# Optimization experiments

Hardware: AMD Instinct MI355X
Metric: run time of the kernel (lower is better)

The kernel has to match this reference:

```python
import jax, jax.numpy as jnp
import numpy as np

H = 256; NH = 8; DH = H // NH; L = 2; B = 32; S = 512; FIN = 199; A = 4


def _ln(x, g, b):
    m = jnp.mean(x, -1, keepdims=True)
    v = jnp.mean((x - m) ** 2, -1, keepdims=True)
    return (x - m) / jnp.sqrt(v + 1e-5) * g + b


def _grn(x, fc1w, fc1b, fc2w, fc2b, gw, gb, ggw, ggb, lg, lb):
    # GatedResidualNetwork, input_dim == output_dim so no skip layer, no context
    h = jax.nn.elu(x @ fc1w + fc1b)
    h = jax.nn.elu(h @ fc2w + fc2b)
    g = (h @ gw + gb) * jax.nn.sigmoid(h @ ggw + ggb)  # GLU
    return _ln(g + x, lg, lb)


def _attn(h, wq, bq, wk, bk, wv, bv, wo, bo):
    b, s, _ = h.shape
    q = (h @ wq + bq).reshape(b, s, NH, DH)
    k = (h @ wk + bk).reshape(b, s, NH, DH)
    v = (h @ wv + bv).reshape(b, s, NH, DH)
    scores = jnp.einsum('bqhd,bkhd->bhqk', q, k) / jnp.sqrt(jnp.float32(DH))
    mask = jnp.triu(jnp.ones((s, s), dtype=bool), 1)  # causal: mask strictly-future
    scores = jnp.where(mask, -jnp.inf, scores)
    aw = jax.nn.softmax(scores, axis=-1)
    ctx = jnp.einsum('bhqk,bkhd->bqhd', aw, v).reshape(b, s, H)
    return ctx @ wo + bo, aw


def _pe(s, d):
    pos = jnp.arange(s, dtype=jnp.float32)[:, None]
    div = jnp.exp(jnp.arange(0, d, 2, dtype=jnp.float32) * (-jnp.log(10000.0) / d))
    pe = jnp.zeros((s, d), dtype=jnp.float32)
    pe = pe.at[:, 0::2].set(jnp.sin(pos * div)).at[:, 1::2].set(jnp.cos(pos * div))
    return pe


def setup_inputs():
    key = jax.random.key(0)
    ks = iter(jax.random.split(key, 80))
    def nrm(shape, sc=0.02):
        return (jax.random.normal(next(ks), shape) * sc).astype(jnp.float32)
    d = {}
    d['x'] = jax.random.normal(next(ks), (B, S, FIN), dtype=jnp.float32)
    d['time_features'] = jax.random.normal(next(ks), (B, S, 3), dtype=jnp.float32)
    d['fp_w'] = nrm((FIN, H)); d['fp_b'] = jnp.zeros((H,), jnp.float32)
    d['tp_w'] = nrm((3, H));   d['tp_b'] = jnp.zeros((H,), jnp.float32)
    d['ip_w'] = nrm((H, H));   d['ip_b'] = jnp.zeros((H,), jnp.float32)
    for nm in ['wq', 'wk', 'wv', 'wo']:
        d[nm] = nrm((L, H, H))
    for nm in ['bq', 'bk', 'bv', 'bo']:
        d[nm] = jnp.zeros((L, H), jnp.float32)
    d['ln_g'] = jnp.ones((L, H), jnp.float32); d['ln_b'] = jnp.zeros((L, H), jnp.float32)
    for nm in ['g_fc1w', 'g_fc2w', 'g_gw', 'g_ggw']:
        d[nm] = nrm((L, H, H))
    for nm in ['g_fc1b', 'g_fc2b', 'g_gb', 'g_ggb']:
        d[nm] = jnp.zeros((L, H), jnp.float32)
    d['g_lg'] = jnp.ones((L, H), jnp.float32); d['g_lb'] = jnp.zeros((L, H), jnp.float32)
    for nm in ['f_fc1w', 'f_fc2w', 'f_gw', 'f_ggw']:
        d[nm] = nrm((H, H))
    for nm in ['f_fc1b', 'f_fc2b', 'f_gb', 'f_ggb']:
        d[nm] = jnp.zeros((H,), jnp.float32)
    d['f_lg'] = jnp.ones((H,), jnp.float32); d['f_lb'] = jnp.zeros((H,), jnp.float32)
    d['out_w'] = nrm((H, A)); d['out_b'] = jnp.zeros((A,), jnp.float32)
    return d


def reference(x, time_features, fp_w, fp_b, tp_w, tp_b, ip_w, ip_b,
              wq, bq, wk, bk, wv, bv, wo, bo, ln_g, ln_b,
              g_fc1w, g_fc1b, g_fc2w, g_fc2b, g_gw, g_gb, g_ggw, g_ggb, g_lg, g_lb,
              f_fc1w, f_fc1b, f_fc2w, f_fc2b, f_gw, f_gb, f_ggw, f_ggb, f_lg, f_lb,
              out_w, out_b):
    s = x.shape[1]
    hidden = (x @ fp_w + fp_b) + (time_features @ tp_w + tp_b)
    hidden = hidden @ ip_w + ip_b
    hidden = hidden + _pe(s, H)[None]
    aw = None
    for i in range(L):
        ao, aw = _attn(hidden, wq[i], bq[i], wk[i], bk[i], wv[i], bv[i], wo[i], bo[i])
        hidden = _ln(hidden + ao, ln_g[i], ln_b[i])
        hidden = _grn(hidden, g_fc1w[i], g_fc1b[i], g_fc2w[i], g_fc2b[i],
                      g_gw[i], g_gb[i], g_ggw[i], g_ggb[i], g_lg[i], g_lb[i])
    hidden = _grn(hidden, f_fc1w, f_fc1b, f_fc2w, f_fc2b, f_gw, f_gb, f_ggw, f_ggb, f_lg, f_lb)
    final = hidden[:, -1, :]
    logits = final @ out_w + out_b  # [B, A], one column per target asset
    return (logits, aw)
```

## Files before the change

kernel.cpp:

```cpp
#include <hip/hip_runtime.h>
#include <hip/hip_fp16.h>
#include <math.h>
#include <cstddef>

#define H 256
#define NH 8
#define DH 32
#define LAYERS 2
#define BB 32
#define SS 512
#define FINDIM 199
#define AA 4
#define T_TOK (BB*SS)
#define KIN 224
#define TPB 64

typedef unsigned short u16;
typedef unsigned int u32;
typedef __attribute__((ext_vector_type(8))) short short8;
typedef __attribute__((ext_vector_type(4))) float f4;

__device__ __forceinline__ float b2f(u16 v){
  unsigned u = ((unsigned)v) << 16;
  return __builtin_bit_cast(float, u);
}
__device__ __forceinline__ u16 f2b(float f){
  unsigned u = __builtin_bit_cast(unsigned, f);
  unsigned r = (u + 0x7fffu + ((u >> 16) & 1u)) >> 16;
  return (u16)r;
}
__device__ __forceinline__ float wave_sum(float v){
  #pragma unroll
  for (int mk=1; mk<64; mk<<=1) v += __shfl_xor(v, mk, 64);
  return v;
}

#define GLD_LDS16(g, l) \
  __builtin_amdgcn_global_load_lds((const __attribute__((address_space(1))) void*)(g), \
                                   (__attribute__((address_space(3))) void*)(l), 16, 0, 0)

#define SA (KIN+8)
#define SY (H+8)

template<int KC, int WK>
__device__ __forceinline__ void stage_acc64(
    const u16* Xl, int sx, const u16* __restrict__ Wt,
    int r0, int c0, int l16, int lq, f4 acc[2][4])
{
  #pragma unroll
  for (int mi=0;mi<2;mi++)
    #pragma unroll
    for (int ni=0;ni<4;ni++) acc[mi][ni] = (f4){0.f,0.f,0.f,0.f};
  #pragma unroll
  for (int kc=0;kc<KC;kc++){
    short8 af[2], bf[4];
    #pragma unroll
    for (int mi=0;mi<2;mi++)
      af[mi] = *(const short8*)&Xl[(r0 + mi*16 + l16)*sx + kc*32 + lq*8];
    #pragma unroll
    for (int ni=0;ni<4;ni++)
      bf[ni] = *(const short8*)(Wt + (size_t)(c0 + ni*16 + l16)*WK + kc*32 + lq*8);
    #pragma unroll
    for (int mi=0;mi<2;mi++)
      #pragma unroll
      for (int ni=0;ni<4;ni++)
        acc[mi][ni] = __builtin_amdgcn_mfma_f32_16x16x32_bf16(af[mi], bf[ni], acc[mi][ni], 0,0,0);
  }
}

template<int DO_ELU>
__device__ __forceinline__ void stage_store64(
    f4 acc[2][4], const float* __restrict__ bias,
    int r0, int c0, int l16, int lq, u16* Yl, int sy)
{
  #pragma unroll
  for (int ni=0;ni<4;ni++){
    int col = c0 + ni*16 + l16;
    float bc = bias[col];
    #pragma unroll
    for (int mi=0;mi<2;mi++){
      #pragma unroll
      for (int r=0;r<4;r++){
        int row = r0 + mi*16 + lq*4 + r;
        float v = acc[mi][ni][r] + bc;
        if (DO_ELU) v = v > 0.f ? v : expm1f(v);
        Yl[row*sy + col] = f2b(v);
      }
    }
  }
}

__device__ __forceinline__ void tile_load64(const u16* g, u16* Yl, int sy, int t){
  #pragma unroll
  for (int j=0;j<4;j++){
    int u = t + j*512;
    int row = u >> 5, cu = u & 31;
    *(short8*)&Yl[row*sy + cu*8] = *(const short8*)(g + (size_t)row*H + cu*8);
  }
}

template<int WB>
__device__ __forceinline__ void tile_ln64(
    u16* Yl, int sy, const float* __restrict__ g, const float* __restrict__ b,
    u16* out, int t)
{
  int w = t >> 6, lane = t & 63;
  #pragma unroll
  for (int rr=0;rr<8;rr++){
    int row = w*8 + rr;
    float xv[4];
    #pragma unroll
    for (int j=0;j<4;j++) xv[j] = b2f(Yl[row*sy + lane*4 + j]);
    float s=0.f, ss=0.f;
    #pragma unroll
    for (int j=0;j<4;j++){ s += xv[j]; ss += xv[j]*xv[j]; }
    s = wave_sum(s); ss = wave_sum(ss);
    float mean = s * (1.0f/H);
    float var  = ss * (1.0f/H) - mean*mean;
    float rstd = rsqrtf(var + 1e-5f);
    ushort4 o;
    int col = lane*4;
    o.x = f2b((xv[0]-mean)*rstd*g[col+0] + b[col+0]);
    o.y = f2b((xv[1]-mean)*rstd*g[col+1] + b[col+1]);
    o.z = f2b((xv[2]-mean)*rstd*g[col+2] + b[col+2]);
    o.w = f2b((xv[3]-mean)*rstd*g[col+3] + b[col+3]);
    *(ushort4*)(out + (size_t)row*H + col) = o;
    if (WB && row == 63) *(ushort4*)(Yl + row*sy + col) = o;
  }
}

struct WPtrs { const float* p[21]; };

__global__ __launch_bounds__(256) void wconv_kernel(WPtrs wp, u16* __restrict__ dst){
  __shared__ float tl[64][65];
  int mb = blockIdx.x >> 4, tile = blockIdx.x & 15;
  int k0 = (tile >> 2) * 64, n0 = (tile & 3) * 64;
  const float* src = wp.p[mb];
  int t = threadIdx.x;
  int r = t >> 4, cg = t & 15;
  #pragma unroll
  for (int p4=0;p4<4;p4++){
    f4 v = *(const f4*)(src + (size_t)(k0 + r + p4*16)*H + n0 + cg*4);
    tl[r+p4*16][cg*4+0]=v[0]; tl[r+p4*16][cg*4+1]=v[1];
    tl[r+p4*16][cg*4+2]=v[2]; tl[r+p4*16][cg*4+3]=v[3];
  }
  __syncthreads();
  u16* db = dst + (size_t)mb*H*H;
  #pragma unroll
  for (int p4=0;p4<4;p4++){
    int rn = r + p4*16;
    ushort4 o;
    o.x = f2b(tl[cg*4+0][rn]); o.y = f2b(tl[cg*4+1][rn]);
    o.z = f2b(tl[cg*4+2][rn]); o.w = f2b(tl[cg*4+3][rn]);
    *(ushort4*)(db + (size_t)(n0+rn)*H + k0 + cg*4) = o;
  }
}

__global__ __launch_bounds__(256) void wcat_kernel(
    const float* __restrict__ fp_w, const float* __restrict__ tp_w,
    u16* __restrict__ wcat){
  int idx = blockIdx.x*256 + threadIdx.x;
  if (idx >= 256*KIN) return;
  int n = idx / KIN, k2 = idx % KIN;
  float v = 0.f;
  if (k2 < FINDIM) v = fp_w[(size_t)k2*H + n];
  else if (k2 < FINDIM+3) v = tp_w[(size_t)(k2-FINDIM)*H + n];
  wcat[idx] = f2b(v);
}

__global__ __launch_bounds__(256) void xconv_kernel(
    const float* __restrict__ x, const float* __restrict__ tf,
    u16* __restrict__ ab){
  size_t idx = (size_t)blockIdx.x*256 + threadIdx.x;
  if (idx >= (size_t)T_TOK*KIN) return;
  int tok = idx / KIN, k2 = idx % KIN;
  float v = 0.f;
  if (k2 < FINDIM) v = x[(size_t)tok*FINDIM + k2];
  else if (k2 < FINDIM+3) v = tf[(size_t)tok*3 + (k2-FINDIM)];
  ab[idx] = f2b(v);
}

__global__ __launch_bounds__(512,2) void input_kernel(
    const u16* __restrict__ ab, const u16* __restrict__ wcat,
    const float* __restrict__ fp_b, const float* __restrict__ tp_b,
    const u16* __restrict__ ipw, const float* __restrict__ ip_b,
    u16* __restrict__ hid){
  __shared__ u16 Al[TPB*SA];
  __shared__ u16 Tl[TPB*SY];
  int t = threadIdx.x;
  int tok0 = blockIdx.x * TPB;
  int lane = t & 63, w = t >> 6;
  int l16 = lane & 15, lq = lane >> 4;
  int r0 = (w >> 2) * 32;
  int c0 = (w & 3) * 64;

  #pragma unroll
  for (int j=0;j<4;j++){
    int u = t + j*512;
    if (u < 1792){
      int row = u / 28, cu = u % 28;
      *(short8*)&Al[row*SA + cu*8] = *(const short8*)(ab + (size_t)(tok0+row)*KIN + cu*8);
    }
  }
  __syncthreads();

  f4 acc[2][4];
  stage_acc64<7, KIN>(Al, SA, wcat, r0, c0, l16, lq, acc);
  #pragma unroll
  for (int ni=0;ni<4;ni++){
    int col = c0 + ni*16 + l16;
    float bc = fp_b[col] + tp_b[col];
    #pragma unroll
    for (int mi=0;mi<2;mi++)
      #pragma unroll
      for (int r=0;r<4;r++){
        int row = r0 + mi*16 + lq*4 + r;
        Tl[row*SY + col] = f2b(acc[mi][ni][r] + bc);
      }
  }
  __syncthreads();

  stage_acc64<8, H>(Tl, SY, ipw, r0, c0, l16, lq, acc);
  #pragma unroll
  for (int ni=0;ni<4;ni++){
    int col = c0 + ni*16 + l16;
    float bc = ip_b[col];
    int ii = col >> 1;
    float div = __expf((float)(2*ii) * -0.03597789207803197f);
    #pragma unroll
    for (int mi=0;mi<2;mi++)
      #pragma unroll
      for (int r=0;r<4;r++){
        int row = r0 + mi*16 + lq*4 + r;
        int s = (tok0 + row) & (SS-1);
        float arg = (float)s * div;
        float pe = (col & 1) ? cosf(arg) : sinf(arg);
        hid[(size_t)(tok0+row)*H + col] = f2b(acc[mi][ni][r] + bc + pe);
      }
  }
}

__global__ __launch_bounds__(512,2) void oproj_ln_kernel(
    const u16* __restrict__ ctx, u16* __restrict__ hid,
    const u16* __restrict__ wo, const float* __restrict__ bo,
    const float* __restrict__ g, const float* __restrict__ b){
  __shared__ u16 Xl[TPB*SY];
  __shared__ u16 Rl[TPB*SY];
  int t = threadIdx.x;
  int tok0 = blockIdx.x * TPB;
  int lane = t & 63, w = t >> 6;
  int l16 = lane & 15, lq = lane >> 4;
  int r0 = (w >> 2) * 32;
  int c0 = (w & 3) * 64;
  u16* hb = hid + (size_t)tok0*H;

  tile_load64(ctx + (size_t)tok0*H, Xl, SY, t);
  tile_load64(hb, Rl, SY, t);
  __syncthreads();

  f4 acc[2][4];
  stage_acc64<8, H>(Xl, SY, wo, r0, c0, l16, lq, acc);
  __syncthreads();
  #pragma unroll
  for (int ni=0;ni<4;ni++){
    int col = c0 + ni*16 + l16;
    float bc = bo[col];
    #pragma unroll
    for (int mi=0;mi<2;mi++)
      #pragma unroll
      for (int r=0;r<4;r++){
        int row = r0 + mi*16 + lq*4 + r;
        float y = acc[mi][ni][r] + bc + b2f(Rl[row*SY + col]);
        Xl[row*SY + col] = f2b(y);
      }
  }
  __syncthreads();
  tile_ln64<0>(Xl, SY, g, b, hb, t);
}

template<int LOGITS>
__global__ __launch_bounds__(512,2) void grn_kernel(
    u16* __restrict__ hid,
    const u16* __restrict__ fc1, const u16* __restrict__ fc2,
    const u16* __restrict__ gw,  const u16* __restrict__ ggw,
    const float* __restrict__ b1, const float* __restrict__ b2,
    const float* __restrict__ gb, const float* __restrict__ ggb,
    const float* __restrict__ lg, const float* __restrict__ lb,
    const float* __restrict__ ow, const float* __restrict__ ob,
    float* __restrict__ lout){
  __shared__ u16 Xa[TPB*SY];
  __shared__ u16 Xb[TPB*SY];
  int t = threadIdx.x;
  int tok0 = blockIdx.x * TPB;
  int lane = t & 63, w = t >> 6;
  int l16 = lane & 15, lq = lane >> 4;
  int r0 = (w >> 2) * 32;
  int c0 = (w & 3) * 64;
  u16* hb = hid + (size_t)tok0*H;

  tile_load64(hb, Xa, SY, t);
  __syncthreads();

  f4 acc[2][4];
  stage_acc64<8, H>(Xa, SY, fc1, r0, c0, l16, lq, acc);
  stage_store64<1>(acc, b1, r0, c0, l16, lq, Xb, SY);
  __syncthreads();
  stage_acc64<8, H>(Xb, SY, fc2, r0, c0, l16, lq, acc);
  __syncthreads();
  stage_store64<1>(acc, b2, r0, c0, l16, lq, Xb, SY);
  __syncthreads();

  stage_acc64<8, H>(Xb, SY, ggw, r0, c0, l16, lq, acc);
  u32 sgp[2][4][2];
  #pragma unroll
  for (int mi=0;mi<2;mi++)
    #pragma unroll
    for (int ni=0;ni<4;ni++){
      float bc = ggb[c0 + ni*16 + l16];
      float s0 = 1.0f/(1.0f + __expf(-(acc[mi][ni][0]+bc)));
      float s1 = 1.0f/(1.0f + __expf(-(acc[mi][ni][1]+bc)));
      float s2 = 1.0f/(1.0f + __expf(-(acc[mi][ni][2]+bc)));
      float s3 = 1.0f/(1.0f + __expf(-(acc[mi][ni][3]+bc)));
      sgp[mi][ni][0] = __builtin_bit_cast(u32, __floats2half2_rn(s0, s1));
      sgp[mi][ni][1] = __builtin_bit_cast(u32, __floats2half2_rn(s2, s3));
    }

  stage_acc64<8, H>(Xb, SY, gw, r0, c0, l16, lq, acc);
  __syncthreads();
  #pragma unroll
  for (int ni=0;ni<4;ni++){
    int col = c0 + ni*16 + l16;
    float bc = gb[col];
    #pragma unroll
    for (int mi=0;mi<2;mi++){
      float2 s01 = __half22float2(__builtin_bit_cast(__half2, sgp[mi][ni][0]));
      float2 s23 = __half22float2(__builtin_bit_cast(__half2, sgp[mi][ni][1]));
      float sv[4] = {s01.x, s01.y, s23.x, s23.y};
      #pragma unroll
      for (int r=0;r<4;r++){
        int row = r0 + mi*16 + lq*4 + r;
        float y = (acc[mi][ni][r] + bc) * sv[r] + b2f(Xa[row*SY + col]);
        Xb[row*SY + col] = f2b(y);
      }
    }
  }
  __syncthreads();
  tile_ln64<LOGITS>(Xb, SY, lg, lb, hb, t);

  if (LOGITS){
    if ((tok0 & (SS-1)) == SS - TPB){
      __syncthreads();
      if (t < 64){
        int bidx = tok0 >> 9;
        float a0=0.f, a1=0.f, a2=0.f, a3=0.f;
        #pragma unroll
        for (int j=0;j<4;j++){
          int k = t*4 + j;
          float xv = b2f(Xb[63*SY + k]);
          f4 wr = *(const f4*)(ow + (size_t)k*AA);
          a0 = fmaf(xv, wr[0], a0);
          a1 = fmaf(xv, wr[1], a1);
          a2 = fmaf(xv, wr[2], a2);
          a3 = fmaf(xv, wr[3], a3);
        }
        a0 = wave_sum(a0); a1 = wave_sum(a1);
        a2 = wave_sum(a2); a3 = wave_sum(a3);
        if (t == 0){
          lout[bidx*AA+0] = a0 + ob[0];
          lout[bidx*AA+1] = a1 + ob[1];
          lout[bidx*AA+2] = a2 + ob[2];
          lout[bidx*AA+3] = a3 + ob[3];
        }
      }
    }
  }
}

struct GemmJob  { const u16* Wt; const float* bias; u16* C; };
struct GemmBatch{ GemmJob j[3]; };

__global__ __launch_bounds__(256) void gemm_bf16(
    const u16* __restrict__ A, GemmBatch jb) {
  __shared__ u16 smem[128*64 + 64*64];
  u16* As  = smem;
  u16* Wsm = smem + 128*64;
  const GemmJob job = jb.j[blockIdx.z];
  const u16* Wt = job.Wt;
  int t = threadIdx.x;
  int m0 = blockIdx.x * 128;
  int n0 = blockIdx.y * 64;
  int lane = t & 63, w = t >> 6;
  int wr = (w >> 1) * 64;
  int wc = (w & 1) * 32;
  int l16 = lane & 15, lq = lane >> 4;

  f4 acc[4][2];
  #pragma unroll
  for (int mi=0;mi<4;mi++)
    #pragma unroll
    for (int ni=0;ni<2;ni++) acc[mi][ni] = (f4){0.f,0.f,0.f,0.f};

  for (int k0=0;k0<256;k0+=64){
    #pragma unroll
    for (int ja=0;ja<4;ja++){
      int ub = (w*4 + ja)*64;
      int u  = ub + lane;
      int m  = u >> 3, c = u & 7, kx = c ^ (m & 7);
      const u16* g = A + (size_t)(m0+m)*H + k0 + kx*8;
      GLD_LDS16(g, As + (size_t)ub*8);
    }
    #pragma unroll
    for (int jb2=0;jb2<2;jb2++){
      int ub = (w*2 + jb2)*64;
      int u  = ub + lane;
      int n  = u >> 3, c = u & 7, kx = c ^ (n & 7);
      const u16* g = Wt + (size_t)(n0+n)*H + k0 + kx*8;
      GLD_LDS16(g, Wsm + (size_t)ub*8);
    }
    __syncthreads();
    #pragma unroll
    for (int kc=0;kc<2;kc++){
      short8 af[4], bf[2];
      int kx = kc*4 + lq;
      #pragma unroll
      for (int mi=0;mi<4;mi++){
        int m = wr + mi*16 + l16;
        int un = (m<<3) | (kx ^ (m&7));
        af[mi] = *(short8*)&As[un*8];
      }
      #pragma unroll
      for (int ni=0;ni<2;ni++){
        int n = wc + ni*16 + l16;
        int un = (n<<3) | (kx ^ (n&7));
        bf[ni] = *(short8*)&Wsm[un*8];
      }
      #pragma unroll
      for (int mi=0;mi<4;mi++)
        #pragma unroll
        for (int ni=0;ni<2;ni++)
          acc[mi][ni] = __builtin_amdgcn_mfma_f32_16x16x32_bf16(af[mi], bf[ni], acc[mi][ni], 0,0,0);
    }
    __syncthreads();
  }

  u16* Cl = smem;
  #pragma unroll
  for (int ni=0;ni<2;ni++){
    int coll = wc + ni*16 + l16;
    float bcol = job.bias[n0 + coll];
    #pragma unroll
    for (int mi=0;mi<4;mi++){
      #pragma unroll
      for (int r=0;r<4;r++){
        int rowl = wr + mi*16 + lq*4 + r;
        Cl[rowl*68 + coll] = f2b(acc[mi][ni][r] + bcol);
      }
    }
  }
  __syncthreads();
  #pragma unroll
  for (int q2=0;q2<4;q2++){
    int u = q2*256 + t;
    int row = u >> 3, cu = u & 7;
    short8 val = *(short8*)&Cl[row*68 + cu*8];
    *(short8*)(job.C + (size_t)(m0+row)*H + n0 + cu*8) = val;
  }
}

template<int WRITE_AW>
__global__ __launch_bounds__(256) void attn_kernel(
    const u16* __restrict__ q, const u16* __restrict__ k,
    const u16* __restrict__ v, float* __restrict__ aw,
    u16* __restrict__ ctx) {
  __shared__ u16 Vt[DH][SS+8];
  __shared__ u16 Plds[4][16][72];
  int t  = threadIdx.x;
  int qt = blockIdx.x;
  int bh = blockIdx.y;
  int b  = bh >> 3, h = bh & 7;
  int lane = t & 63, w = t >> 6;
  int l16 = lane & 15, lq = lane >> 4;
  const float scale = 0.17677669529663687f;

  int nrows = (qt+1)*64;
  for (int kk = t; kk < nrows; kk += 256){
    const u16* vp = v + ((size_t)(b*SS + kk))*H + h*DH;
    short8 r0v = *(const short8*)(vp);
    short8 r1v = *(const short8*)(vp+8);
    short8 r2v = *(const short8*)(vp+16);
    short8 r3v = *(const short8*)(vp+24);
    #pragma unroll
    for (int j=0;j<8;j++){
      Vt[j][kk]    = (u16)r0v[j];
      Vt[8+j][kk]  = (u16)r1v[j];
      Vt[16+j][kk] = (u16)r2v[j];
      Vt[24+j][kk] = (u16)r3v[j];
    }
  }
  __syncthreads();

  {
    int qr0 = qt*64 + w*16;
    int KT  = qt*4 + w + 1;
    short8 af = *(const short8*)(q + ((size_t)(b*SS + qr0 + l16))*H + h*DH + lq*8);

    float l[4] = {0.f,0.f,0.f,0.f};
    f4 o[2] = {(f4){0.f,0.f,0.f,0.f}, (f4){0.f,0.f,0.f,0.f}};
    u32 pk0[32], pk1[32];

    #pragma unroll
    for (int c8=0;c8<8;c8++){
      if (c8*4 < KT){
        #pragma unroll
        for (int j=0;j<4;j++){
          int kt = c8*4 + j;
          float p[4] = {0.f,0.f,0.f,0.f};
          if (kt < KT){
            short8 bfr = *(const short8*)(k + ((size_t)(b*SS + kt*16 + l16))*H + h*DH + lq*8);
            f4 cc = (f4){0.f,0.f,0.f,0.f};
            cc = __builtin_amdgcn_mfma_f32_16x16x32_bf16(af, bfr, cc, 0,0,0);
            int col = kt*16 + l16;
            #pragma unroll
            for (int i=0;i<4;i++){
              int qi = qr0 + lq*4 + i;
              float sc = (col <= qi) ? cc[i]*scale : -3.0e38f;
              p[i] = __expf(sc);
              l[i] += p[i];
            }
          }
          u16 pb[4];
          #pragma unroll
          for (int i=0;i<4;i++) pb[i] = f2b(p[i]);
          if (WRITE_AW){
            pk0[kt] = (u32)pb[0] | ((u32)pb[1] << 16);
            pk1[kt] = (u32)pb[2] | ((u32)pb[3] << 16);
          }
          #pragma unroll
          for (int i=0;i<4;i++) Plds[w][lq*4+i][j*16+l16] = pb[i];
        }
        #pragma unroll
        for (int kc=0;kc<2;kc++){
          short8 pa = *(short8*)&Plds[w][l16][kc*32 + lq*8];
          #pragma unroll
          for (int dt=0;dt<2;dt++){
            short8 vb = *(const short8*)&Vt[dt*16 + l16][c8*64 + kc*32 + lq*8];
            o[dt] = __builtin_amdgcn_mfma_f32_16x16x32_bf16(pa, vb, o[dt], 0,0,0);
          }
        }
      }
    }

    #pragma unroll
    for (int i=0;i<4;i++){
      #pragma unroll
      for (int mk=1; mk<16; mk<<=1) l[i] += __shfl_xor(l[i], mk, 64);
    }
    float inv[4];
    #pragma unroll
    for (int i=0;i<4;i++) inv[i] = 1.0f / l[i];

    if (WRITE_AW){
      float* ab = aw + (size_t)bh*SS*SS;
      #pragma unroll
      for (int kt=0;kt<32;kt++){
        if (kt < KT){
          int col = kt*16 + l16;
          float pv[4] = { b2f((u16)pk0[kt]), b2f((u16)(pk0[kt]>>16)),
                          b2f((u16)pk1[kt]), b2f((u16)(pk1[kt]>>16)) };
          #pragma unroll
          for (int i=0;i<4;i++){
            int qi = qr0 + lq*4 + i;
            float val = (col <= qi) ? pv[i]*inv[i] : 0.f;
            __builtin_nontemporal_store(val, &ab[(size_t)qi*SS + col]);
          }
        }
      }
      int c4base = KT*4;
      f4 z = (f4){0.f,0.f,0.f,0.f};
      #pragma unroll
      for (int ri=0;ri<4;ri++){
        int row = qr0 + ri*4 + lq;
        for (int j=l16; j < 128 - c4base; j += 16)
          __builtin_nontemporal_store(z, (f4*)&ab[(size_t)row*SS + (size_t)(c4base+j)*4]);
      }
    }

    #pragma unroll
    for (int dt=0;dt<2;dt++){
      #pragma unroll
      for (int i=0;i<4;i++){
        int row = qr0 + lq*4 + i;
        ctx[((size_t)(b*SS + row))*H + h*DH + dt*16 + l16] = f2b(o[dt][i]*inv[i]);
      }
    }
  }
}

extern "C" void kernel_launch(void* const* d_in, const int* in_sizes, int n_in,
                              void* d_out, int out_size, void* d_ws, size_t ws_size,
                              hipStream_t stream){
  (void)in_sizes; (void)n_in; (void)out_size; (void)ws_size;
  const float* x      = (const float*)d_in[0];
  const float* tf     = (const float*)d_in[1];
  const float* fp_w   = (const float*)d_in[2];
  const float* fp_b   = (const float*)d_in[3];
  const float* tp_w   = (const float*)d_in[4];
  const float* tp_b   = (const float*)d_in[5];
  const float* ip_w   = (const float*)d_in[6];
  const float* ip_b   = (const float*)d_in[7];
  const float* wq     = (const float*)d_in[8];
  const float* wk     = (const float*)d_in[9];
  const float* wv     = (const float*)d_in[10];
  const float* wo     = (const float*)d_in[11];
  const float* bq     = (const float*)d_in[12];
  const float* bk     = (const float*)d_in[13];
  const float* bv     = (const float*)d_in[14];
  const float* bo     = (const float*)d_in[15];
  const float* ln_g   = (const float*)d_in[16];
  const float* ln_b   = (const float*)d_in[17];
  const float* g_fc1w = (const float*)d_in[18];
  const float* g_fc2w = (const float*)d_in[19];
  const float* g_gw   = (const float*)d_in[20];
  const float* g_ggw  = (const float*)d_in[21];
  const float* g_fc1b = (const float*)d_in[22];
  const float* g_fc2b = (const float*)d_in[23];
  const float* g_gb   = (const float*)d_in[24];
  const float* g_ggb  = (const float*)d_in[25];
  const float* g_lg   = (const float*)d_in[26];
  const float* g_lb   = (const float*)d_in[27];
  const float* f_fc1w = (const float*)d_in[28];
  const float* f_fc2w = (const float*)d_in[29];
  const float* f_gw   = (const float*)d_in[30];
  const float* f_ggw  = (const float*)d_in[31];
  const float* f_fc1b = (const float*)d_in[32];
  const float* f_fc2b = (const float*)d_in[33];
  const float* f_gb   = (const float*)d_in[34];
  const float* f_ggb  = (const float*)d_in[35];
  const float* f_lg   = (const float*)d_in[36];
  const float* f_lb   = (const float*)d_in[37];
  const float* out_w  = (const float*)d_in[38];
  const float* out_b  = (const float*)d_in[39];

  float* logits = (float*)d_out;
  float* aw     = logits + BB*AA;

  u16* wts = (u16*)d_ws;
  const size_t WMAT = (size_t)H*H;
  u16* wcat = wts  + 21*WMAT;
  u16* abuf = wcat + (size_t)H*KIN;
  u16* hid  = abuf + (size_t)T_TOK*KIN;
  size_t BUF = (size_t)T_TOK * H;
  u16* buf1 = hid  + BUF;
  u16* buf2 = buf1 + BUF;
  u16* buf3 = buf2 + BUF;

  WPtrs wp;
  wp.p[0]  = ip_w;
  wp.p[1]  = wq;        wp.p[2]  = wq + WMAT;
  wp.p[3]  = wk;        wp.p[4]  = wk + WMAT;
  wp.p[5]  = wv;        wp.p[6]  = wv + WMAT;
  wp.p[7]  = wo;        wp.p[8]  = wo + WMAT;
  wp.p[9]  = g_fc1w;    wp.p[10] = g_fc1w + WMAT;
  wp.p[11] = g_fc2w;    wp.p[12] = g_fc2w + WMAT;
  wp.p[13] = g_gw;      wp.p[14] = g_gw + WMAT;
  wp.p[15] = g_ggw;     wp.p[16] = g_ggw + WMAT;
  wp.p[17] = f_fc1w;    wp.p[18] = f_fc2w;
  wp.p[19] = f_gw;      wp.p[20] = f_ggw;
  const int WT_IP=0, WT_Q=1, WT_K=3, WT_V=5, WT_O=7,
            WT_FC1=9, WT_FC2=11, WT_GW=13, WT_GGW=15,
            WT_FFC1=17, WT_FFC2=18, WT_FGW=19, WT_FGGW=20;

  dim3 b256(256), b512(512);
  dim3 gAttn(8, BB*NH);
  dim3 gTok(T_TOK/TPB);

  wconv_kernel<<<21*16, b256, 0, stream>>>(wp, wts);
  wcat_kernel<<<(H*KIN+255)/256, b256, 0, stream>>>(fp_w, tp_w, wcat);
  xconv_kernel<<<(T_TOK*KIN+255)/256, b256, 0, stream>>>(x, tf, abuf);
  input_kernel<<<gTok, b512, 0, stream>>>(abuf, wcat, fp_b, tp_b,
                                          wts + (size_t)WT_IP*WMAT, ip_b, hid);

  for (int i=0;i<LAYERS;i++){
    const size_t BOFF = (size_t)i*H;
    GemmBatch gb;
    gb.j[0] = { wts + (size_t)(WT_Q+i)*WMAT, bq+BOFF, buf1 };
    gb.j[1] = { wts + (size_t)(WT_K+i)*WMAT, bk+BOFF, buf2 };
    gb.j[2] = { wts + (size_t)(WT_V+i)*WMAT, bv+BOFF, buf3 };
    gemm_bf16<<<dim3(T_TOK/128, H/64, 3), b256, 0, stream>>>(hid, gb);
    if (i == LAYERS-1)
      attn_kernel<1><<<gAttn, b256, 0, stream>>>(buf1, buf2, buf3, aw, buf1);
    else
      attn_kernel<0><<<gAttn, b256, 0, stream>>>(buf1, buf2, buf3, aw, buf1);
    oproj_ln_kernel<<<gTok, b512, 0, stream>>>(buf1, hid,
        wts + (size_t)(WT_O+i)*WMAT, bo+BOFF, ln_g+BOFF, ln_b+BOFF);
    grn_kernel<0><<<gTok, b512, 0, stream>>>(hid,
        wts + (size_t)(WT_FC1+i)*WMAT, wts + (size_t)(WT_FC2+i)*WMAT,
        wts + (size_t)(WT_GW+i)*WMAT,  wts + (size_t)(WT_GGW+i)*WMAT,
        g_fc1b+BOFF, g_fc2b+BOFF, g_gb+BOFF, g_ggb+BOFF,
        g_lg+BOFF, g_lb+BOFF, nullptr, nullptr, nullptr);
  }

  grn_kernel<1><<<gTok, b512, 0, stream>>>(hid,
      wts + (size_t)WT_FFC1*WMAT, wts + (size_t)WT_FFC2*WMAT,
      wts + (size_t)WT_FGW*WMAT,  wts + (size_t)WT_FGGW*WMAT,
      f_fc1b, f_fc2b, f_gb, f_ggb, f_lg, f_lb,
      out_w, out_b, logits);
}
```

Before: 678.6 us.

## Fuse prepass kernels, merge out-proj+LN with GRN, vectorize attention stores

New measurement: 980.5 us. 44.5% more time.

```diff
diff --git a/kernel.cpp b/kernel.cpp
--- a/kernel.cpp
+++ b/kernel.cpp
@@ -14,6 +14,7 @@
 #define T_TOK (BB*SS)
 #define KIN 224
 #define TPB 64
+#define XBLK ((T_TOK*KIN)/256)
 
 typedef unsigned short u16;
 typedef unsigned int u32;
@@ -33,6 +34,18 @@
   #pragma unroll
   for (int mk=1; mk<64; mk<<=1) v += __shfl_xor(v, mk, 64);
   return v;
+}
+
+__device__ __forceinline__ void quad_transpose(float a[4], int j2){
+  float tv;
+  tv = __shfl_xor((j2&1)? a[0] : a[1], 1, 64);
+  if (j2&1) a[0]=tv; else a[1]=tv;
+  tv = __shfl_xor((j2&1)? a[2] : a[3], 1, 64);
+  if (j2&1) a[2]=tv; else a[3]=tv;
+  tv = __shfl_xor((j2&2)? a[0] : a[2], 2, 64);
+  if (j2&2) a[0]=tv; else a[2]=tv;
+  tv = __shfl_xor((j2&2)? a[1] : a[3], 2, 64);
+  if (j2&2) a[1]=tv; else a[3]=tv;
 }
 
 #define GLD_LDS16(g, l) \
@@ -129,55 +142,82 @@
   }
 }
 
+__device__ __forceinline__ void tile_ln64_lds(
+    const u16* Yl, int sy, const float* __restrict__ g, const float* __restrict__ b,
+    u16* Ol, int t)
+{
+  int w = t >> 6, lane = t & 63;
+  #pragma unroll
+  for (int rr=0;rr<8;rr++){
+    int row = w*8 + rr;
+    float xv[4];
+    #pragma unroll
+    for (int j=0;j<4;j++) xv[j] = b2f(Yl[row*sy + lane*4 + j]);
+    float s=0.f, ss=0.f;
+    #pragma unroll
+    for (int j=0;j<4;j++){ s += xv[j]; ss += xv[j]*xv[j]; }
+    s = wave_sum(s); ss = wave_sum(ss);
+    float mean = s * (1.0f/H);
+    float var  = ss * (1.0f/H) - mean*mean;
+    float rstd = rsqrtf(var + 1e-5f);
+    ushort4 o;
+    int col = lane*4;
+    o.x = f2b((xv[0]-mean)*rstd*g[col+0] + b[col+0]);
+    o.y = f2b((xv[1]-mean)*rstd*g[col+1] + b[col+1]);
+    o.z = f2b((xv[2]-mean)*rstd*g[col+2] + b[col+2]);
+    o.w = f2b((xv[3]-mean)*rstd*g[col+3] + b[col+3]);
+    *(ushort4*)(Ol + (size_t)row*sy + col) = o;
+  }
+}
+
 struct WPtrs { const float* p[21]; };
 
-__global__ __launch_bounds__(256) void wconv_kernel(WPtrs wp, u16* __restrict__ dst){
+__global__ __launch_bounds__(256) void prepass_kernel(
+    WPtrs wp, u16* __restrict__ wts_dst,
+    const float* __restrict__ x, const float* __restrict__ tf, u16* __restrict__ ab,
+    const float* __restrict__ fp_w, const float* __restrict__ tp_w,
+    u16* __restrict__ wcat)
+{
   __shared__ float tl[64][65];
-  int mb = blockIdx.x >> 4, tile = blockIdx.x & 15;
-  int k0 = (tile >> 2) * 64, n0 = (tile & 3) * 64;
-  const float* src = wp.p[mb];
+  int bid = blockIdx.x;
   int t = threadIdx.x;
-  int r = t >> 4, cg = t & 15;
-  #pragma unroll
-  for (int p4=0;p4<4;p4++){
-    f4 v = *(const f4*)(src + (size_t)(k0 + r + p4*16)*H + n0 + cg*4);
-    tl[r+p4*16][cg*4+0]=v[0]; tl[r+p4*16][cg*4+1]=v[1];
-    tl[r+p4*16][cg*4+2]=v[2]; tl[r+p4*16][cg*4+3]=v[3];
-  }
-  __syncthreads();
-  u16* db = dst + (size_t)mb*H*H;
-  #pragma unroll
-  for (int p4=0;p4<4;p4++){
-    int rn = r + p4*16;
-    ushort4 o;
-    o.x = f2b(tl[cg*4+0][rn]); o.y = f2b(tl[cg*4+1][rn]);
-    o.z = f2b(tl[cg*4+2][rn]); o.w = f2b(tl[cg*4+3][rn]);
-    *(ushort4*)(db + (size_t)(n0+rn)*H + k0 + cg*4) = o;
-  }
-}
-
-__global__ __launch_bounds__(256) void wcat_kernel(
-    const float* __restrict__ fp_w, const float* __restrict__ tp_w,
-    u16* __restrict__ wcat){
-  int idx = blockIdx.x*256 + threadIdx.x;
-  if (idx >= 256*KIN) return;
-  int n = idx / KIN, k2 = idx % KIN;
-  float v = 0.f;
-  if (k2 < FINDIM) v = fp_w[(size_t)k2*H + n];
-  else if (k2 < FINDIM+3) v = tp_w[(size_t)(k2-FINDIM)*H + n];
-  wcat[idx] = f2b(v);
-}
-
-__global__ __launch_bounds__(256) void xconv_kernel(
-    const float* __restrict__ x, const float* __restrict__ tf,
-    u16* __restrict__ ab){
-  size_t idx = (size_t)blockIdx.x*256 + threadIdx.x;
-  if (idx >= (size_t)T_TOK*KIN) return;
-  int tok = idx / KIN, k2 = idx % KIN;
-  float v = 0.f;
-  if (k2 < FINDIM) v = x[(size_t)tok*FINDIM + k2];
-  else if (k2 < FINDIM+3) v = tf[(size_t)tok*3 + (k2-FINDIM)];
-  ab[idx] = f2b(v);
+  if (bid < XBLK){
+    size_t idx = (size_t)bid*256 + t;
+    int tok = idx / KIN, k2 = idx % KIN;
+    float v = 0.f;
+    if (k2 < FINDIM) v = x[(size_t)tok*FINDIM + k2];
+    else if (k2 < FINDIM+3) v = tf[(size_t)tok*3 + (k2-FINDIM)];
+    ab[idx] = f2b(v);
+  } else if (bid < XBLK + 336){
+    int bb2 = bid - XBLK;
+    int mb = bb2 >> 4, tile = bb2 & 15;
+    int k0 = (tile >> 2) * 64, n0 = (tile & 3) * 64;
+    const float* src = wp.p[mb];
+    int r = t >> 4, cg = t & 15;
+    #pragma unroll
+    for (int p4=0;p4<4;p4++){
+      f4 v = *(const f4*)(src + (size_t)(k0 + r + p4*16)*H + n0 + cg*4);
+      tl[r+p4*16][cg*4+0]=v[0]; tl[r+p4*16][cg*4+1]=v[1];
+      tl[r+p4*16][cg*4+2]=v[2]; tl[r+p4*16][cg*4+3]=v[3];
+    }
+    __syncthreads();
+    u16* db = wts_dst + (size_t)mb*H*H;
+    #pragma unroll
+    for (int p4=0;p4<4;p4++){
+      int rn = r + p4*16;
+      ushort4 o;
+      o.x = f2b(tl[cg*4+0][rn]); o.y = f2b(tl[cg*4+1][rn]);
+      o.z = f2b(tl[cg*4+2][rn]); o.w = f2b(tl[cg*4+3][rn]);
+      *(ushort4*)(db + (size_t)(n0+rn)*H + k0 + cg*4) = o;
+    }
+  } else {
+    int idx = (bid - XBLK - 336)*256 + t;
+    int n = idx / KIN, k2 = idx % KIN;
+    float v = 0.f;
+    if (k2 < FINDIM) v = fp_w[(size_t)k2*H + n];
+    else if (k2 < FINDIM+3) v = tp_w[(size_t)(k2-FINDIM)*H + n];
+    wcat[idx] = f2b(v);
+  }
 }
 
 __global__ __launch_bounds__(512,2) void input_kernel(
@@ -240,12 +280,18 @@
   }
 }
 
-__global__ __launch_bounds__(512,2) void oproj_ln_kernel(
+__global__ __launch_bounds__(512,2) void post_kernel(
     const u16* __restrict__ ctx, u16* __restrict__ hid,
     const u16* __restrict__ wo, const float* __restrict__ bo,
-    const float* __restrict__ g, const float* __restrict__ b){
-  __shared__ u16 Xl[TPB*SY];
-  __shared__ u16 Rl[TPB*SY];
+    const float* __restrict__ g0, const float* __restrict__ b0,
+    const u16* __restrict__ fc1, const u16* __restrict__ fc2,
+    const u16* __restrict__ gw,  const u16* __restrict__ ggw,
+    const float* __restrict__ b1, const float* __restrict__ b2,
+    const float* __restrict__ gb, const float* __restrict__ ggb,
+    const float* __restrict__ lg, const float* __restrict__ lb)
+{
+  __shared__ u16 Xa[TPB*SY];
+  __shared__ u16 Xb[TPB*SY];
   int t = threadIdx.x;
   int tok0 = blockIdx.x * TPB;
   int lane = t & 63, w = t >> 6;
@@ -254,12 +300,12 @@
   int c0 = (w & 3) * 64;
   u16* hb = hid + (size_t)tok0*H;
 
-  tile_load64(ctx + (size_t)tok0*H, Xl, SY, t);
-  tile_load64(hb, Rl, SY, t);
+  tile_load64(ctx + (size_t)tok0*H, Xa, SY, t);
+  tile_load64(hb, Xb, SY, t);
   __syncthreads();
 
   f4 acc[2][4];
-  stage_acc64<8, H>(Xl, SY, wo, r0, c0, l16, lq, acc);
+  stage_acc64<8, H>(Xa, SY, wo, r0, c0, l16, lq, acc);
   __syncthreads();
   #pragma unroll
   for (int ni=0;ni<4;ni++){
@@ -270,12 +316,57 @@
       #pragma unroll
       for (int r=0;r<4;r++){
         int row = r0 + mi*16 + lq*4 + r;
-        float y = acc[mi][ni][r] + bc + b2f(Rl[row*SY + col]);
-        Xl[row*SY + col] = f2b(y);
-      }
-  }
-  __syncthreads();
-  tile_ln64<0>(Xl, SY, g, b, hb, t);
+        Xa[row*SY + col] = f2b(acc[mi][ni][r] + bc + b2f(Xb[row*SY + col]));
+      }
+  }
+  __syncthreads();
+  tile_ln64_lds(Xa, SY, g0, b0, Xb, t);
+  __syncthreads();
+
+  stage_acc64<8, H>(Xb, SY, fc1, r0, c0, l16, lq, acc);
+  stage_store64<1>(acc, b1, r0, c0, l16, lq, Xa, SY);
+  __syncthreads();
+  stage_acc64<8, H>(Xa, SY, fc2, r0, c0, l16, lq, acc);
+  __syncthreads();
+  stage_store64<1>(acc, b2, r0, c0, l16, lq, Xa, SY);
+  __syncthreads();
+
+  stage_acc64<8, H>(Xa, SY, ggw, r0, c0, l16, lq, acc);
+  u32 sgp[2][4][2];
+  #pragma unroll
+  for (int mi=0;mi<2;mi++)
+    #pragma unroll
+    for (int ni=0;ni<4;ni++){
+      float bc = ggb[c0 + ni*16 + l16];
+      float s0 = 1.0f/(1.0f + __expf(-(acc[mi][ni][0]+bc)));
+      float s1 = 1.0f/(1.0f + __expf(-(acc[mi][ni][1]+bc)));
+      float s2 = 1.0f/(1.0f + __expf(-(acc[mi][ni][2]+bc)));
+      float s3 = 1.0f/(1.0f + __expf(-(acc[mi][ni][3]+bc)));
+      sgp[mi][ni][0] = __builtin_bit_cast(u32, __floats2half2_rn(s0, s1));
+      sgp[mi][ni][1] = __builtin_bit_cast(u32, __floats2half2_rn(s2, s3));
+    }
+
+  stage_acc64<8, H>(Xa, SY, gw, r0, c0, l16, lq, acc);
+  __syncthreads();
+  #pragma unroll
+  for (int ni=0;ni<4;ni++){
+    int col = c0 + ni*16 + l16;
+    float bc = gb[col];
+    #pragma unroll
+    for (int mi=0;mi<2;mi++){
+      float2 s01 = __half22float2(__builtin_bit_cast(__half2, sgp[mi][ni][0]));
+      float2 s23 = __half22float2(__builtin_bit_cast(__half2, sgp[mi][ni][1]));
+      float sv[4] = {s01.x, s01.y, s23.x, s23.y};
+      #pragma unroll
+      for (int r=0;r<4;r++){
+        int row = r0 + mi*16 + lq*4 + r;
+        float y = (acc[mi][ni][r] + bc) * sv[r] + b2f(Xb[row*SY + col]);
+        Xa[row*SY + col] = f2b(y);
+      }
+    }
+  }
+  __syncthreads();
+  tile_ln64<0>(Xa, SY, lg, lb, hb, t);
 }
 
 template<int LOGITS>
@@ -480,6 +571,7 @@
   int b  = bh >> 3, h = bh & 7;
   int lane = t & 63, w = t >> 6;
   int l16 = lane & 15, lq = lane >> 4;
+  int j2 = l16 & 3;
   const float scale = 0.17677669529663687f;
 
   int nrows = (qt+1)*64;
@@ -565,14 +657,16 @@
       for (int kt=0;kt<32;kt++){
         if (kt < KT){
           int col = kt*16 + l16;
-          float pv[4] = { b2f((u16)pk0[kt]), b2f((u16)(pk0[kt]>>16)),
-                          b2f((u16)pk1[kt]), b2f((u16)(pk1[kt]>>16)) };
-          #pragma unroll
-          for (int i=0;i<4;i++){
-            int qi = qr0 + lq*4 + i;
-            float val = (col <= qi) ? pv[i]*inv[i] : 0.f;
-            __builtin_nontemporal_store(val, &ab[(size_t)qi*SS + col]);
-          }
+          float aa[4];
+          aa[0] = (col <= qr0+lq*4+0) ? b2f((u16)pk0[kt])*inv[0] : 0.f;
+          aa[1] = (col <= qr0+lq*4+1) ? b2f((u16)(pk0[kt]>>16))*inv[1] : 0.f;
+          aa[2] = (col <= qr0+lq*4+2) ? b2f((u16)pk1[kt])*inv[2] : 0.f;
+          aa[3] = (col <= qr0+lq*4+3) ? b2f((u16)(pk1[kt]>>16))*inv[3] : 0.f;
+          quad_transpose(aa, j2);
+          f4 vv = {aa[0],aa[1],aa[2],aa[3]};
+          int row = qr0 + lq*4 + j2;
+          int colbase = kt*16 + (l16 & ~3);
+          __builtin_nontemporal_store(vv, (f4*)&ab[(size_t)row*SS + colbase]);
         }
       }
       int c4base = KT*4;
@@ -587,11 +681,14 @@
 
     #pragma unroll
     for (int dt=0;dt<2;dt++){
-      #pragma unroll
-      for (int i=0;i<4;i++){
-        int row = qr0 + lq*4 + i;
-        ctx[((size_t)(b*SS + row))*H + h*DH + dt*16 + l16] = f2b(o[dt][i]*inv[i]);
-      }
+      float aa[4];
+      #pragma unroll
+      for (int i=0;i<4;i++) aa[i] = o[dt][i]*inv[i];
+      quad_transpose(aa, j2);
+      ushort4 pk;
+      pk.x = f2b(aa[0]); pk.y = f2b(aa[1]); pk.z = f2b(aa[2]); pk.w = f2b(aa[3]);
+      int row = qr0 + lq*4 + j2;
+      *(ushort4*)(ctx + ((size_t)(b*SS + row))*H + h*DH + dt*16 + (l16 & ~3)) = pk;
     }
   }
 }
@@ -674,9 +771,8 @@
   dim3 gAttn(8, BB*NH);
   dim3 gTok(T_TOK/TPB);
 
-  wconv_kernel<<<21*16, b256, 0, stream>>>(wp, wts);
-  wcat_kernel<<<(H*KIN+255)/256, b256, 0, stream>>>(fp_w, tp_w, wcat);
-  xconv_kernel<<<(T_TOK*KIN+255)/256, b256, 0, stream>>>(x, tf, abuf);
+  prepass_kernel<<<XBLK + 336 + 224, b256, 0, stream>>>(
+      wp, wts, x, tf, abuf, fp_w, tp_w, wcat);
   input_kernel<<<gTok, b512, 0, stream>>>(abuf, wcat, fp_b, tp_b,
                                           wts + (size_t)WT_IP*WMAT, ip_b, hid);
 
@@ -691,13 +787,12 @@
       attn_kernel<1><<<gAttn, b256, 0, stream>>>(buf1, buf2, buf3, aw, buf1);
     else
       attn_kernel<0><<<gAttn, b256, 0, stream>>>(buf1, buf2, buf3, aw, buf1);
-    oproj_ln_kernel<<<gTok, b512, 0, stream>>>(buf1, hid,
-        wts + (size_t)(WT_O+i)*WMAT, bo+BOFF, ln_g+BOFF, ln_b+BOFF);
-    grn_kernel<0><<<gTok, b512, 0, stream>>>(hid,
+    post_kernel<<<gTok, b512, 0, stream>>>(buf1, hid,
+        wts + (size_t)(WT_O+i)*WMAT, bo+BOFF, ln_g+BOFF, ln_b+BOFF,
         wts + (size_t)(WT_FC1+i)*WMAT, wts + (size_t)(WT_FC2+i)*WMAT,
         wts + (size_t)(WT_GW+i)*WMAT,  wts + (size_t)(WT_GGW+i)*WMAT,
         g_fc1b+BOFF, g_fc2b+BOFF, g_gb+BOFF, g_ggb+BOFF,
-        g_lg+BOFF, g_lb+BOFF, nullptr, nullptr, nullptr);
+        g_lg+BOFF, g_lb+BOFF);
   }
 
   grn_kernel<1><<<gTok, b512, 0, stream>>>(hid,
```
